# Optimization experiments

Measured on AMD Instinct MI355X. Metric: run time of the kernel, lower is better.

## Reference

```python
import jax, jax.numpy as jnp
import numpy as np

D_MODEL = 256
NUM_HEADS = 8
CURV = 1.0  # Poincare ball curvature c
EPS = 1e-5


def expmap0(v, c):
    # Exponential map at the origin of the Poincare ball.
    sqrt_c = jnp.sqrt(c)
    norm = jnp.sqrt(jnp.clip(jnp.sum(v * v, axis=-1, keepdims=True), 1e-12))
    return jnp.tanh(sqrt_c * norm) * v / (sqrt_c * norm)


def setup_inputs() -> dict:
    key = jax.random.key(0)
    ks = jax.random.split(key, 12)
    B, S, D = 2, 2048, D_MODEL
    s = 1.0 / np.sqrt(D)
    return {
        "x": jax.random.normal(ks[0], (B, S, D), dtype=jnp.float32),
        "Wq": jax.random.normal(ks[1], (D, D), dtype=jnp.float32) * s,
        "bq": jnp.zeros((D,), jnp.float32),
        "Wk": jax.random.normal(ks[2], (D, D), dtype=jnp.float32) * s,
        "bk": jnp.zeros((D,), jnp.float32),
        "Wv": jax.random.normal(ks[3], (D, D), dtype=jnp.float32) * s,
        "bv": jnp.zeros((D,), jnp.float32),
        "Wo": jax.random.normal(ks[4], (D, D), dtype=jnp.float32) * s,
        "bo": jnp.zeros((D,), jnp.float32),
        "Wfc": jax.random.normal(ks[5], (D, D), dtype=jnp.float32) * s,
        "bfc": jnp.zeros((D,), jnp.float32),
    }


def reference(x, Wq, bq, Wk, bk, Wv, bv, Wo, bo, Wfc, bfc):
    B, S, D = x.shape
    H, dh = NUM_HEADS, D // NUM_HEADS
    c = CURV

    def proj(W, b):
        return (x @ W.T + b).reshape(B, S, H, dh).transpose(0, 2, 1, 3)  # [B,H,S,dh]

    q = expmap0(proj(Wq, bq), c)
    k = expmap0(proj(Wk, bk), c)
    v = proj(Wv, bv)

    # Gram quantities; pairwise Poincare distance via closed-form Mobius-add norm.
    qq = jnp.sum(q * q, axis=-1)[..., :, None]          # [B,H,S,1]
    kk = jnp.sum(k * k, axis=-1)[..., None, :]          # [B,H,1,S]
    qk = jnp.einsum("bhsd,bhtd->bhst", q, k)            # [B,H,S,S]

    A = 1.0 - 2.0 * c * qk + c * kk
    Bc = 1.0 - c * qq
    den = 1.0 - 2.0 * c * qk + (c * c) * qq * kk
    num2 = A * A * qq + Bc * Bc * kk - 2.0 * A * Bc * qk  # ||(-q) mobius+ k||^2 * den^2
    n = jnp.sqrt(jnp.clip(num2, 0.0)) / jnp.clip(jnp.abs(den), 1e-12)
    sqrt_c = jnp.sqrt(c)
    dist = (2.0 / sqrt_c) * jnp.arctanh(jnp.clip(sqrt_c * n, 0.0, 1.0 - EPS))

    scores = -dist / np.sqrt(dh)
    attn = jax.nn.softmax(scores, axis=-1)
    out = jnp.einsum("bhst,bhtd->bhsd", attn, v)        # [B,H,S,dh]
    out = out.transpose(0, 2, 1, 3).reshape(B, S, D)
    out = out @ Wo.T + bo
    return out @ Wfc.T + bfc
```

## Files before the change

kernel.cpp:

```cpp
#include <hip/hip_runtime.h>
#include <cstdint>
#include <cstddef>


#define ALPHA 0.17677669529663687f
#define EMIN  -3.1129694f
#define CHI   1.95e-5f

typedef __bf16 bf16x8 __attribute__((ext_vector_type(8)));
typedef float  f32x4  __attribute__((ext_vector_type(4)));

__device__ __forceinline__ float fast_log2(float x) { return __builtin_amdgcn_logf(x); }
__device__ __forceinline__ float fast_exp2(float x) { return __builtin_amdgcn_exp2f(x); }

__device__ __forceinline__ void load_lds16(const void* g, void* l) {
  __builtin_amdgcn_global_load_lds((const __attribute__((address_space(1))) void*)g,
                                   (__attribute__((address_space(3))) void*)l, 16, 0, 0);
}

__global__ __launch_bounds__(256)
void split_all(const float* __restrict__ x, const float* __restrict__ Wq,
               const float* __restrict__ Wk, const float* __restrict__ Wv,
               __bf16* __restrict__ xh, __bf16* __restrict__ xl,
               __bf16* __restrict__ Ws) {
  int g = blockIdx.x * 256 + threadIdx.x;
  const float* src;
  __bf16 *dh, *dl;
  if (g < 131072) {
    src = x + (size_t)g * 8; dh = xh + (size_t)g * 8; dl = xl + (size_t)g * 8;
  } else {
    int e = g - 131072;
    int wsel = e >> 13;
    int inner = (e & 8191) * 8;
    src = (wsel == 0 ? Wq : (wsel == 1 ? Wk : Wv)) + inner;
    dh = Ws + wsel * 131072 + inner;
    dl = Ws + wsel * 131072 + 65536 + inner;
  }
  union { __bf16 h[8]; uint4 u; } ph, pl;
#pragma unroll
  for (int i = 0; i < 2; ++i) {
    float4 v = *(const float4*)(src + i * 4);
    float vv[4] = {v.x, v.y, v.z, v.w};
#pragma unroll
    for (int j = 0; j < 4; ++j) {
      __bf16 hb = (__bf16)vv[j];
      ph.h[i * 4 + j] = hb;
      pl.h[i * 4 + j] = (__bf16)(vv[j] - (float)hb);
    }
  }
  *(uint4*)dh = ph.u;
  *(uint4*)dl = pl.u;
}

__global__ __launch_bounds__(256)
void gemm_qkv_mfma(const __bf16* __restrict__ xh, const __bf16* __restrict__ xl,
                   const __bf16* __restrict__ Ws,
                   const float* __restrict__ bq, const float* __restrict__ bk,
                   const float* __restrict__ bv,
                   float* __restrict__ Qb, float* __restrict__ Kb,
                   float* __restrict__ Vb) {
  const int tid = threadIdx.x, w = tid >> 6, lane = tid & 63;
  const int l15 = lane & 15, lg = lane >> 4;
  const int m0 = blockIdx.x * 64, nb = blockIdx.y;
  const int wsel = nb >> 2;
  const int n256b = (nb & 3) * 64;
  const __bf16* Wh = Ws + wsel * 131072;
  const __bf16* Wl = Wh + 65536;
  const int arow = m0 + w * 16 + l15;
  const __bf16* axh = xh + (size_t)arow * 256 + lg * 8;
  const __bf16* axl = xl + (size_t)arow * 256 + lg * 8;
  f32x4 acc0 = {0,0,0,0}, acc1 = {0,0,0,0}, acc2 = {0,0,0,0}, acc3 = {0,0,0,0};
#pragma unroll
  for (int k0 = 0; k0 < 256; k0 += 32) {
    bf16x8 ah = *(const bf16x8*)(axh + k0);
    bf16x8 al = *(const bf16x8*)(axl + k0);
#pragma unroll
    for (int g = 0; g < 4; ++g) {
      const size_t br = (size_t)(n256b + g * 16 + l15) * 256 + lg * 8 + k0;
      bf16x8 bh = *(const bf16x8*)(Wh + br);
      bf16x8 bl = *(const bf16x8*)(Wl + br);
      f32x4& acc = g == 0 ? acc0 : (g == 1 ? acc1 : (g == 2 ? acc2 : acc3));
      acc = __builtin_amdgcn_mfma_f32_16x16x32_bf16(ah, bh, acc, 0, 0, 0);
      acc = __builtin_amdgcn_mfma_f32_16x16x32_bf16(al, bh, acc, 0, 0, 0);
      acc = __builtin_amdgcn_mfma_f32_16x16x32_bf16(ah, bl, acc, 0, 0, 0);
    }
  }
  const float* bias = wsel == 0 ? bq : (wsel == 1 ? bk : bv);
  float* C = wsel == 0 ? Qb : (wsel == 1 ? Kb : Vb);
#pragma unroll
  for (int g = 0; g < 4; ++g) {
    const f32x4& acc = g == 0 ? acc0 : (g == 1 ? acc1 : (g == 2 ? acc2 : acc3));
    int n256 = n256b + g * 16 + l15;
    float bval = bias[n256];
    int h = n256 >> 5, d = n256 & 31;
#pragma unroll
    for (int r = 0; r < 4; ++r) {
      int m = m0 + w * 16 + lg * 4 + r;
      int b = m >> 11, s = m & 2047;
      C[((size_t)((b << 3) + h) << 16) + (size_t)s * 32 + d] = acc[r] + bval;
    }
  }
}

__global__ __launch_bounds__(256)
void gemm_out_mfma(const __bf16* __restrict__ aoh, const __bf16* __restrict__ aol,
                   const __bf16* __restrict__ Wch, const __bf16* __restrict__ Wcl,
                   const float* __restrict__ bcomb, float* __restrict__ out) {
  const int tid = threadIdx.x, w = tid >> 6, lane = tid & 63;
  const int l15 = lane & 15, lg = lane >> 4;
  const int m0 = blockIdx.x * 64, n0 = blockIdx.y * 64;
  const int arow = m0 + w * 16 + l15;
  const __bf16* axh = aoh + (size_t)arow * 256 + lg * 8;
  const __bf16* axl = aol + (size_t)arow * 256 + lg * 8;
  f32x4 acc0 = {0,0,0,0}, acc1 = {0,0,0,0}, acc2 = {0,0,0,0}, acc3 = {0,0,0,0};
#pragma unroll
  for (int k0 = 0; k0 < 256; k0 += 32) {
    bf16x8 ah = *(const bf16x8*)(axh + k0);
    bf16x8 al = *(const bf16x8*)(axl + k0);
#pragma unroll
    for (int g = 0; g < 4; ++g) {
      const size_t br = (size_t)(n0 + g * 16 + l15) * 256 + lg * 8 + k0;
      bf16x8 bh = *(const bf16x8*)(Wch + br);
      bf16x8 bl = *(const bf16x8*)(Wcl + br);
      f32x4& acc = g == 0 ? acc0 : (g == 1 ? acc1 : (g == 2 ? acc2 : acc3));
      acc = __builtin_amdgcn_mfma_f32_16x16x32_bf16(ah, bh, acc, 0, 0, 0);
      acc = __builtin_amdgcn_mfma_f32_16x16x32_bf16(al, bh, acc, 0, 0, 0);
      acc = __builtin_amdgcn_mfma_f32_16x16x32_bf16(ah, bl, acc, 0, 0, 0);
    }
  }
#pragma unroll
  for (int g = 0; g < 4; ++g) {
    const f32x4& acc = g == 0 ? acc0 : (g == 1 ? acc1 : (g == 2 ? acc2 : acc3));
    int n = n0 + g * 16 + l15;
    float bval = bcomb[n];
#pragma unroll
    for (int r = 0; r < 4; ++r) {
      int m = m0 + w * 16 + lg * 4 + r;
      out[(size_t)m * 256 + n] = acc[r] + bval;
    }
  }
}

__global__ __launch_bounds__(256)
void gemm_nn_small(const float* __restrict__ Afc, const float* __restrict__ Bo,
                   __bf16* __restrict__ Ch, __bf16* __restrict__ Cl) {
  __shared__ float AsT[32][68];
  __shared__ float Bs[32][68];
  const int tid = threadIdx.x;
  const int ty = tid >> 4, tx = tid & 15;
  const int m0 = blockIdx.x * 64;
  const int n0 = blockIdx.y * 64;
  float acc[4][4] = {};
  for (int k0 = 0; k0 < 256; k0 += 32) {
#pragma unroll
    for (int jj = 0; jj < 2; ++jj) {
      int j = tid * 2 + jj;
      {
        int r = j >> 3, c4 = (j & 7) << 2;
        float4 av = *(const float4*)&Afc[(size_t)(m0 + r) * 256 + k0 + c4];
        AsT[c4 + 0][r] = av.x; AsT[c4 + 1][r] = av.y;
        AsT[c4 + 2][r] = av.z; AsT[c4 + 3][r] = av.w;
      }
      {
        int r = j >> 4, c4 = (j & 15) << 2;
        *(float4*)&Bs[r][c4] = *(const float4*)&Bo[(size_t)(k0 + r) * 256 + n0 + c4];
      }
    }
    __syncthreads();
#pragma unroll
    for (int kk = 0; kk < 32; ++kk) {
      float4 a = *(const float4*)&AsT[kk][ty * 4];
      float4 b = *(const float4*)&Bs[kk][tx * 4];
      float av[4] = {a.x, a.y, a.z, a.w};
      float bv[4] = {b.x, b.y, b.z, b.w};
#pragma unroll
      for (int i = 0; i < 4; ++i)
#pragma unroll
        for (int j2 = 0; j2 < 4; ++j2)
          acc[i][j2] = fmaf(av[i], bv[j2], acc[i][j2]);
    }
    __syncthreads();
  }
#pragma unroll
  for (int i = 0; i < 4; ++i) {
    union { __bf16 h[4]; uint2 u; } ph, pl;
#pragma unroll
    for (int j = 0; j < 4; ++j) {
      __bf16 hb = (__bf16)acc[i][j];
      ph.h[j] = hb;
      pl.h[j] = (__bf16)(acc[i][j] - (float)hb);
    }
    size_t off = (size_t)(m0 + ty * 4 + i) * 256 + n0 + tx * 4;
    *(uint2*)(Ch + off) = ph.u;
    *(uint2*)(Cl + off) = pl.u;
  }
}

__global__ __launch_bounds__(256)
void bcomb_k(const float* __restrict__ Wfc, const float* __restrict__ bo,
             const float* __restrict__ bfc, float* __restrict__ bcomb) {
  __shared__ float red[256];
  int r = threadIdx.x >> 4, c = threadIdx.x & 15;
  int row = blockIdx.x * 16 + r;
  float s = 0.0f;
  for (int k = c; k < 256; k += 16) s = fmaf(Wfc[(size_t)row * 256 + k], bo[k], s);
  red[threadIdx.x] = s;
  __syncthreads();
  if (c == 0) {
    float t = 0.0f;
#pragma unroll
    for (int i = 0; i < 16; ++i) t += red[r * 16 + i];
    bcomb[row] = t + bfc[row];
  }
}

__global__ __launch_bounds__(256)
void prep_qk(const float* __restrict__ Qf, const float* __restrict__ Kf,
             __bf16* __restrict__ Qbf, __bf16* __restrict__ Kbf,
             float4* __restrict__ qtab4, float4* __restrict__ ktab4) {
  int idx = blockIdx.x * 256 + threadIdx.x;
  const bool isQ = idx < 32768;
  const int i2 = isQ ? idx : idx - 32768;
  const float* src = (isQ ? Qf : Kf) + (size_t)i2 * 32;
  __bf16* dst = (isQ ? Qbf : Kbf) + (size_t)i2 * 32;
  float v[32];
  float ss = 0.0f;
#pragma unroll
  for (int i = 0; i < 8; ++i) {
    float4 v4 = *(const float4*)&src[i * 4];
    v[i*4+0] = v4.x; v[i*4+1] = v4.y; v[i*4+2] = v4.z; v[i*4+3] = v4.w;
    ss = fmaf(v4.x, v4.x, ss); ss = fmaf(v4.y, v4.y, ss);
    ss = fmaf(v4.z, v4.z, ss); ss = fmaf(v4.w, v4.w, ss);
  }
  ss = fmaxf(ss, 1e-12f);
  float x  = sqrtf(ss);
  float ex = fast_exp2(-2.8853900817779268f * x);
  float opex = 1.0f + ex;
  float th = (1.0f - ex) / opex;
  float sc = th / x;
  float qq = th * th;
  float Bv = 4.0f * ex / (opex * opex);
  float lgB = 2.0f - 2.8853900817779268f * x - 2.0f * fast_log2(opex);
  if (isQ) qtab4[i2] = float4{qq, ALPHA * lgB, Bv, 0.0f};
  else     ktab4[i2] = float4{qq, Bv, ALPHA * lgB, 0.0f};
  union { __bf16 h[8]; uint4 u; } pk;
#pragma unroll
  for (int blk = 0; blk < 4; ++blk) {
#pragma unroll
    for (int j = 0; j < 8; ++j) pk.h[j] = (__bf16)(v[blk * 8 + j] * sc);
    *(uint4*)(dst + blk * 8) = pk.u;
  }
}

__global__ __launch_bounds__(256)
void prep_vt(const float* __restrict__ Vf, __bf16* __restrict__ Vt) {
  int g = blockIdx.x * 256 + threadIdx.x;
  int bh = g >> 13, rem = g & 8191;
  int tb = rem >> 5, dh = rem & 31;
  const float* src = Vf + (((size_t)bh * 2048 + tb * 8) * 32) + dh;
  union { __bf16 h[8]; uint4 u; } pk;
#pragma unroll
  for (int e = 0; e < 8; ++e) pk.h[e] = (__bf16)src[e * 32];
  *(uint4*)(Vt + ((size_t)bh * 32 + dh) * 2048 + tb * 8) = pk.u;
}

__global__ __launch_bounds__(256)
void vsum_k(const __bf16* __restrict__ Vt, float* __restrict__ Vsum) {
  int g = blockIdx.x * 256 + threadIdx.x;
  int bh = g >> 11, rem = g & 2047;
  int t32 = rem >> 5, dh = rem & 31;
  const __bf16* src = Vt + ((size_t)bh * 32 + dh) * 2048 + t32 * 32;
  float s = 0.0f;
#pragma unroll
  for (int i = 0; i < 4; ++i) {
    bf16x8 v = *(const bf16x8*)&src[i * 8];
#pragma unroll
    for (int j = 0; j < 8; ++j) s += (float)v[j];
  }
  Vsum[((size_t)bh * 64 + t32) * 32 + dh] = s;
}

__global__ __launch_bounds__(256)
void attn_mfma(const __bf16* __restrict__ Qbf, const __bf16* __restrict__ Kbf,
               const __bf16* __restrict__ Vt,  const float4* __restrict__ qtab4,
               const float4* __restrict__ ktab4, const float* __restrict__ Vsum,
               float* __restrict__ PN, float* __restrict__ PD) {
  __shared__ __bf16 Kst[2][2048];
  __shared__ float4 Tst[2][64];
  __shared__ __bf16 Pt[4][16][72];
  const int tid = threadIdx.x;
  const int wid = tid >> 6, lane = tid & 63;
  const int l15 = lane & 15, lg = lane >> 4;
  const int tc = blockIdx.y, bh = blockIdx.z;
  const int sblk = blockIdx.x;
  const int s0 = sblk * 64 + wid * 16;

  bf16x8 qfrag = *(const bf16x8*)(Qbf + ((size_t)bh * 2048 + s0 + l15) * 32 + lg * 8);
  float4 qt = qtab4[bh * 2048 + s0 + l15];
  const float qq = qt.x, Bq = qt.z;
  const float eminRow = EMIN - qt.y;
  const float wclipf = (float)(__bf16)fast_exp2(eminRow);
  float wrow[4];
#pragma unroll
  for (int r = 0; r < 4; ++r)
    wrow[r] = (float)(__bf16)fast_exp2(EMIN - qtab4[bh * 2048 + s0 + lg * 4 + r].y);

  const __bf16* Kbase = Kbf + ((size_t)bh << 16);
  const __bf16* Vbase = Vt + ((size_t)bh << 16);
  const float4* Tbase = ktab4 + bh * 2048;
  const float*  VsBase = Vsum + (size_t)bh * 64 * 32;
  __bf16* Pw = &Pt[wid][0][0];

  f32x4 accO0 = {0.f, 0.f, 0.f, 0.f};
  f32x4 accO1 = {0.f, 0.f, 0.f, 0.f};
  float den = 0.0f;
  const f32x4 zero = {0.f, 0.f, 0.f, 0.f};
  const int tbeg = tc * 512;
  const int stag = sblk & 7;

  const int slot = wid * 64 + lane;
  const int gch = slot ^ ((slot >> 2) & 3);

  {
    const int t0 = tbeg + ((stag & 7) << 6);
    load_lds16(Kbase + (size_t)t0 * 32 + gch * 8, &Kst[0][wid * 512]);
    if (wid == 0) load_lds16(Tbase + t0 + lane, &Tst[0][0]);
  }
  int cur = 0;

  for (int i = 0; i < 8; ++i) {
    __syncthreads();
    if (i < 7) {
      const int tn = tbeg + (((i + 1 + stag) & 7) << 6);
      load_lds16(Kbase + (size_t)tn * 32 + gch * 8, &Kst[cur ^ 1][wid * 512]);
      if (wid == 0) load_lds16(Tbase + tn + lane, &Tst[cur ^ 1][0]);
    }
    const int t0 = tbeg + (((i + stag) & 7) << 6);
    const __bf16* Kc = &Kst[cur][0];
    const float4* Tc = &Tst[cur][0];

#pragma unroll
    for (int h = 0; h < 2; ++h) {
      f32x4 S[2];
      bool ok = true;
#pragma unroll
      for (int s2 = 0; s2 < 2; ++s2) {
        const int sub = h * 2 + s2;
        const int R = sub * 16 + l15;
        const int slotR = R * 4 + (lg ^ (R & 3));
        bf16x8 kfrag = *(const bf16x8*)&Kc[slotR * 8];
        f32x4 Sv = __builtin_amdgcn_mfma_f32_16x16x32_bf16(kfrag, qfrag, zero, 0, 0, 0);
        S[s2] = Sv;
        const int tk = sub * 16 + lg * 4;
#pragma unroll
        for (int r = 0; r < 4; ++r) {
          float2 T2 = *(const float2*)&Tc[tk + r];
          float d = fmaf(qq, T2.x, 1.0f) - (Sv[r] + Sv[r]);
          ok &= (fmaf(-CHI, d, Bq * T2.y) <= 0.0f);
        }
      }
      if (__all((int)ok)) {
        const int ti32 = (t0 >> 5) + h;
        float vsA = VsBase[ti32 * 32 + l15];
        float vsB = VsBase[ti32 * 32 + 16 + l15];
        den += 8.0f * wclipf;
#pragma unroll
        for (int r = 0; r < 4; ++r) {
          accO0[r] = fmaf(wrow[r], vsA, accO0[r]);
          accO1[r] = fmaf(wrow[r], vsB, accO1[r]);
        }
      } else {
#pragma unroll
        for (int s2 = 0; s2 < 2; ++s2) {
          const int sub = h * 2 + s2;
          const int tk = sub * 16 + lg * 4;
          f32x4 Sv = S[s2];
          float w[4];
#pragma unroll
          for (int r = 0; r < 4; ++r) {
            float4 T = Tc[tk + r];
            float qk2 = Sv[r] + Sv[r];
            float u = (qq + T.x) - qk2;
            float d = fmaf(qq, T.x, 1.0f) - qk2;
            float p = fmaxf(u * d, 0.0f);
            float sq = sqrtf(p);
            float m = fmaf(2.0f, sq, u + d);
            float e = fmaf(-ALPHA, fast_log2(m), T.z);
            e = fmaxf(e, eminRow);
            w[r] = fast_exp2(e);
          }
          den += (w[0] + w[1]) + (w[2] + w[3]);
          union { __bf16 hh[4]; uint2 u2; } pk;
          pk.hh[0] = (__bf16)w[0]; pk.hh[1] = (__bf16)w[1];
          pk.hh[2] = (__bf16)w[2]; pk.hh[3] = (__bf16)w[3];
          *(uint2*)&Pw[l15 * 72 + sub * 16 + lg * 4] = pk.u2;
        }
        bf16x8 pfrag = *(const bf16x8*)&Pw[l15 * 72 + h * 32 + lg * 8];
        bf16x8 v0 = *(const bf16x8*)(Vbase + (size_t)l15 * 2048 + t0 + h * 32 + lg * 8);
        bf16x8 v1 = *(const bf16x8*)(Vbase + (size_t)(16 + l15) * 2048 + t0 + h * 32 + lg * 8);
        accO0 = __builtin_amdgcn_mfma_f32_16x16x32_bf16(pfrag, v0, accO0, 0, 0, 0);
        accO1 = __builtin_amdgcn_mfma_f32_16x16x32_bf16(pfrag, v1, accO1, 0, 0, 0);
      }
    }
    cur ^= 1;
  }
  den += __shfl_xor(den, 16);
  den += __shfl_xor(den, 32);
  size_t pbase = ((size_t)tc * 16 + bh) * 2048;
  if (lg == 0) PD[pbase + s0 + l15] = den;
#pragma unroll
  for (int r = 0; r < 4; ++r) {
    int sl = lg * 4 + r;
    size_t row = (pbase + s0 + sl) * 32;
    PN[row + l15]      = accO0[r];
    PN[row + 16 + l15] = accO1[r];
  }
}

__global__ __launch_bounds__(256)
void combine4(const float* __restrict__ PN, const float* __restrict__ PD,
              __bf16* __restrict__ AOh, __bf16* __restrict__ AOl) {
  int idx = blockIdx.x * 256 + threadIdx.x;
  int bh = idx >> 11, s = idx & 2047;
  int b = bh >> 3, h = bh & 7;
  float den = 0.0f;
#pragma unroll
  for (int c = 0; c < 4; ++c) den += PD[((size_t)c * 16 + bh) * 2048 + s];
  float r = 1.0f / den;
  size_t ob = ((size_t)b * 2048 + s) * 256 + h * 32;
#pragma unroll
  for (int i = 0; i < 8; ++i) {
    float4 sum = {0.0f, 0.0f, 0.0f, 0.0f};
#pragma unroll
    for (int c = 0; c < 4; ++c) {
      float4 v = *(const float4*)&PN[((((size_t)c * 16 + bh) * 2048 + s) * 32) + i * 4];
      sum.x += v.x; sum.y += v.y; sum.z += v.z; sum.w += v.w;
    }
    float vv[4] = {sum.x * r, sum.y * r, sum.z * r, sum.w * r};
    union { __bf16 h4[4]; uint2 u; } ph, pl;
#pragma unroll
    for (int j = 0; j < 4; ++j) {
      __bf16 hb = (__bf16)vv[j];
      ph.h4[j] = hb;
      pl.h4[j] = (__bf16)(vv[j] - (float)hb);
    }
    *(uint2*)(AOh + ob + i * 4) = ph.u;
    *(uint2*)(AOl + ob + i * 4) = pl.u;
  }
}

extern "C" void kernel_launch(void* const* d_in, const int* in_sizes, int n_in,
                              void* d_out, int out_size, void* d_ws, size_t ws_size,
                              hipStream_t stream) {
  const float* x   = (const float*)d_in[0];
  const float* Wq  = (const float*)d_in[1];
  const float* bq  = (const float*)d_in[2];
  const float* Wk  = (const float*)d_in[3];
  const float* bk  = (const float*)d_in[4];
  const float* Wv  = (const float*)d_in[5];
  const float* bv  = (const float*)d_in[6];
  const float* Wo  = (const float*)d_in[7];
  const float* bo  = (const float*)d_in[8];
  const float* Wfc = (const float*)d_in[9];
  const float* bfc = (const float*)d_in[10];

  float* ws = (float*)d_ws;
  float* Qb  = ws;
  float* Kb  = ws + (1 << 20);
  float* Vb  = ws + (2 << 20);
  __bf16* Qbf = (__bf16*)(ws + (3 << 20));
  __bf16* Kbf = (__bf16*)(ws + (3 << 20) + (1 << 19));
  __bf16* Vtb = (__bf16*)(ws + (4 << 20));
  float4* qtab4 = (float4*)(ws + (4 << 20) + (1 << 19));
  float4* ktab4 = (float4*)(ws + (4 << 20) + (1 << 19) + (1 << 17));
  float*  Vsum  = ws + (4 << 20) + (1 << 19) + (2 << 17);
  __bf16* Wch   = (__bf16*)(ws + (4 << 20) + (1 << 19) + (2 << 17) + (1 << 15));
  __bf16* Wcl   = Wch + 65536;
  float*  bcomb = ws + (4 << 20) + (1 << 19) + (2 << 17) + (1 << 15) + (1 << 16);
  __bf16* xh = (__bf16*)(ws + (5 << 20));
  __bf16* xl = (__bf16*)(ws + (5 << 20) + (1 << 19));
  __bf16* Wsplit = (__bf16*)(ws + (6 << 20));
  float* PN = ws + (6 << 20) + (1 << 18);
  float* PD = PN + (4 << 20);
  __bf16* AOh = (__bf16*)ws;
  __bf16* AOl = (__bf16*)(ws + (1 << 19));

  dim3 blk(256);
  split_all<<<dim3(608), blk, 0, stream>>>(x, Wq, Wk, Wv, xh, xl, Wsplit);
  gemm_qkv_mfma<<<dim3(64, 12), blk, 0, stream>>>(xh, xl, Wsplit, bq, bk, bv, Qb, Kb, Vb);
  prep_qk<<<dim3(256), blk, 0, stream>>>(Qb, Kb, Qbf, Kbf, qtab4, ktab4);
  prep_vt<<<dim3(512), blk, 0, stream>>>(Vb, Vtb);
  vsum_k<<<dim3(128), blk, 0, stream>>>(Vtb, Vsum);
  gemm_nn_small<<<dim3(4, 4), blk, 0, stream>>>(Wfc, Wo, Wch, Wcl);
  bcomb_k<<<dim3(16), blk, 0, stream>>>(Wfc, bo, bfc, bcomb);
  attn_mfma<<<dim3(32, 4, 16), blk, 0, stream>>>(Qbf, Kbf, Vtb, qtab4, ktab4, Vsum, PN, PD);
  combine4<<<dim3(128), blk, 0, stream>>>(PN, PD, AOh, AOl);
  gemm_out_mfma<<<dim3(64, 4), blk, 0, stream>>>(AOh, AOl, Wch, Wcl, bcomb, (float*)d_out);
}
```

Before: 123.3 us.

## Merge prep kernels and use per-head key bounds for skip test

After: 109.6 us. 1.13x faster.

```diff
diff --git a/kernel.cpp b/kernel.cpp
--- a/kernel.cpp
+++ b/kernel.cpp
@@ -6,6 +6,7 @@
 #define ALPHA 0.17677669529663687f
 #define EMIN  -3.1129694f
 #define CHI   1.95e-5f
+#define NEG_INV_2CHI -25641.026f
 
 typedef __bf16 bf16x8 __attribute__((ext_vector_type(8)));
 typedef float  f32x4  __attribute__((ext_vector_type(4)));
@@ -19,37 +20,107 @@
 }
 
 __global__ __launch_bounds__(256)
-void split_all(const float* __restrict__ x, const float* __restrict__ Wq,
-               const float* __restrict__ Wk, const float* __restrict__ Wv,
-               __bf16* __restrict__ xh, __bf16* __restrict__ xl,
-               __bf16* __restrict__ Ws) {
-  int g = blockIdx.x * 256 + threadIdx.x;
-  const float* src;
-  __bf16 *dh, *dl;
-  if (g < 131072) {
-    src = x + (size_t)g * 8; dh = xh + (size_t)g * 8; dl = xl + (size_t)g * 8;
+void k1_misc(const float* __restrict__ x,   const float* __restrict__ Wq,
+             const float* __restrict__ Wk,  const float* __restrict__ Wv,
+             const float* __restrict__ Wfc, const float* __restrict__ Wo,
+             const float* __restrict__ bo,  const float* __restrict__ bfc,
+             __bf16* __restrict__ xh, __bf16* __restrict__ xl,
+             __bf16* __restrict__ Ws, __bf16* __restrict__ Wch,
+             __bf16* __restrict__ Wcl, float* __restrict__ bcomb) {
+  __shared__ float sh[2 * 32 * 68];
+  const int bx = blockIdx.x, tid = threadIdx.x;
+  if (bx < 16) {
+    float (*AsT)[68] = (float(*)[68])sh;
+    float (*Bs)[68]  = (float(*)[68])(sh + 32 * 68);
+    const int ty = tid >> 4, tx = tid & 15;
+    const int m0 = (bx >> 2) * 64, n0 = (bx & 3) * 64;
+    float acc[4][4] = {};
+    for (int k0 = 0; k0 < 256; k0 += 32) {
+#pragma unroll
+      for (int jj = 0; jj < 2; ++jj) {
+        int j = tid * 2 + jj;
+        {
+          int r = j >> 3, c4 = (j & 7) << 2;
+          float4 av = *(const float4*)&Wfc[(size_t)(m0 + r) * 256 + k0 + c4];
+          AsT[c4 + 0][r] = av.x; AsT[c4 + 1][r] = av.y;
+          AsT[c4 + 2][r] = av.z; AsT[c4 + 3][r] = av.w;
+        }
+        {
+          int r = j >> 4, c4 = (j & 15) << 2;
+          *(float4*)&Bs[r][c4] = *(const float4*)&Wo[(size_t)(k0 + r) * 256 + n0 + c4];
+        }
+      }
+      __syncthreads();
+#pragma unroll
+      for (int kk = 0; kk < 32; ++kk) {
+        float4 a = *(const float4*)&AsT[kk][ty * 4];
+        float4 b = *(const float4*)&Bs[kk][tx * 4];
+        float av[4] = {a.x, a.y, a.z, a.w};
+        float bv[4] = {b.x, b.y, b.z, b.w};
+#pragma unroll
+        for (int i = 0; i < 4; ++i)
+#pragma unroll
+          for (int j2 = 0; j2 < 4; ++j2)
+            acc[i][j2] = fmaf(av[i], bv[j2], acc[i][j2]);
+      }
+      __syncthreads();
+    }
+#pragma unroll
+    for (int i = 0; i < 4; ++i) {
+      union { __bf16 h[4]; uint2 u; } ph, pl;
+#pragma unroll
+      for (int j = 0; j < 4; ++j) {
+        __bf16 hb = (__bf16)acc[i][j];
+        ph.h[j] = hb;
+        pl.h[j] = (__bf16)(acc[i][j] - (float)hb);
+      }
+      size_t off = (size_t)(m0 + ty * 4 + i) * 256 + n0 + tx * 4;
+      *(uint2*)(Wch + off) = ph.u;
+      *(uint2*)(Wcl + off) = pl.u;
+    }
+  } else if (bx < 32) {
+    float* red = sh;
+    int r = tid >> 4, c = tid & 15;
+    int row = (bx - 16) * 16 + r;
+    float s = 0.0f;
+    for (int k = c; k < 256; k += 16) s = fmaf(Wfc[(size_t)row * 256 + k], bo[k], s);
+    red[tid] = s;
+    __syncthreads();
+    if (c == 0) {
+      float t = 0.0f;
+#pragma unroll
+      for (int i = 0; i < 16; ++i) t += red[r * 16 + i];
+      bcomb[row] = t + bfc[row];
+    }
   } else {
-    int e = g - 131072;
-    int wsel = e >> 13;
-    int inner = (e & 8191) * 8;
-    src = (wsel == 0 ? Wq : (wsel == 1 ? Wk : Wv)) + inner;
-    dh = Ws + wsel * 131072 + inner;
-    dl = Ws + wsel * 131072 + 65536 + inner;
-  }
-  union { __bf16 h[8]; uint4 u; } ph, pl;
-#pragma unroll
-  for (int i = 0; i < 2; ++i) {
-    float4 v = *(const float4*)(src + i * 4);
-    float vv[4] = {v.x, v.y, v.z, v.w};
-#pragma unroll
-    for (int j = 0; j < 4; ++j) {
-      __bf16 hb = (__bf16)vv[j];
-      ph.h[i * 4 + j] = hb;
-      pl.h[i * 4 + j] = (__bf16)(vv[j] - (float)hb);
-    }
-  }
-  *(uint4*)dh = ph.u;
-  *(uint4*)dl = pl.u;
+    int g = (bx - 32) * 256 + tid;
+    const float* src;
+    __bf16 *dh, *dl;
+    if (g < 131072) {
+      src = x + (size_t)g * 8; dh = xh + (size_t)g * 8; dl = xl + (size_t)g * 8;
+    } else {
+      int e = g - 131072;
+      int wsel = e >> 13;
+      int inner = (e & 8191) * 8;
+      src = (wsel == 0 ? Wq : (wsel == 1 ? Wk : Wv)) + inner;
+      dh = Ws + wsel * 131072 + inner;
+      dl = Ws + wsel * 131072 + 65536 + inner;
+    }
+    union { __bf16 h[8]; uint4 u; } ph, pl;
+#pragma unroll
+    for (int i = 0; i < 2; ++i) {
+      float4 v = *(const float4*)(src + i * 4);
+      float vv[4] = {v.x, v.y, v.z, v.w};
+#pragma unroll
+      for (int j = 0; j < 4; ++j) {
+        __bf16 hb = (__bf16)vv[j];
+        ph.h[i * 4 + j] = hb;
+        pl.h[i * 4 + j] = (__bf16)(vv[j] - (float)hb);
+      }
+    }
+    *(uint4*)dh = ph.u;
+    *(uint4*)dl = pl.u;
+  }
 }
 
 __global__ __launch_bounds__(256)
@@ -103,190 +174,87 @@
 }
 
 __global__ __launch_bounds__(256)
-void gemm_out_mfma(const __bf16* __restrict__ aoh, const __bf16* __restrict__ aol,
-                   const __bf16* __restrict__ Wch, const __bf16* __restrict__ Wcl,
-                   const float* __restrict__ bcomb, float* __restrict__ out) {
-  const int tid = threadIdx.x, w = tid >> 6, lane = tid & 63;
-  const int l15 = lane & 15, lg = lane >> 4;
-  const int m0 = blockIdx.x * 64, n0 = blockIdx.y * 64;
-  const int arow = m0 + w * 16 + l15;
-  const __bf16* axh = aoh + (size_t)arow * 256 + lg * 8;
-  const __bf16* axl = aol + (size_t)arow * 256 + lg * 8;
-  f32x4 acc0 = {0,0,0,0}, acc1 = {0,0,0,0}, acc2 = {0,0,0,0}, acc3 = {0,0,0,0};
-#pragma unroll
-  for (int k0 = 0; k0 < 256; k0 += 32) {
-    bf16x8 ah = *(const bf16x8*)(axh + k0);
-    bf16x8 al = *(const bf16x8*)(axl + k0);
-#pragma unroll
-    for (int g = 0; g < 4; ++g) {
-      const size_t br = (size_t)(n0 + g * 16 + l15) * 256 + lg * 8 + k0;
-      bf16x8 bh = *(const bf16x8*)(Wch + br);
-      bf16x8 bl = *(const bf16x8*)(Wcl + br);
-      f32x4& acc = g == 0 ? acc0 : (g == 1 ? acc1 : (g == 2 ? acc2 : acc3));
-      acc = __builtin_amdgcn_mfma_f32_16x16x32_bf16(ah, bh, acc, 0, 0, 0);
-      acc = __builtin_amdgcn_mfma_f32_16x16x32_bf16(al, bh, acc, 0, 0, 0);
-      acc = __builtin_amdgcn_mfma_f32_16x16x32_bf16(ah, bl, acc, 0, 0, 0);
-    }
-  }
-#pragma unroll
-  for (int g = 0; g < 4; ++g) {
-    const f32x4& acc = g == 0 ? acc0 : (g == 1 ? acc1 : (g == 2 ? acc2 : acc3));
-    int n = n0 + g * 16 + l15;
-    float bval = bcomb[n];
-#pragma unroll
-    for (int r = 0; r < 4; ++r) {
-      int m = m0 + w * 16 + lg * 4 + r;
-      out[(size_t)m * 256 + n] = acc[r] + bval;
-    }
-  }
-}
-
-__global__ __launch_bounds__(256)
-void gemm_nn_small(const float* __restrict__ Afc, const float* __restrict__ Bo,
-                   __bf16* __restrict__ Ch, __bf16* __restrict__ Cl) {
-  __shared__ float AsT[32][68];
-  __shared__ float Bs[32][68];
-  const int tid = threadIdx.x;
-  const int ty = tid >> 4, tx = tid & 15;
-  const int m0 = blockIdx.x * 64;
-  const int n0 = blockIdx.y * 64;
-  float acc[4][4] = {};
-  for (int k0 = 0; k0 < 256; k0 += 32) {
-#pragma unroll
-    for (int jj = 0; jj < 2; ++jj) {
-      int j = tid * 2 + jj;
-      {
-        int r = j >> 3, c4 = (j & 7) << 2;
-        float4 av = *(const float4*)&Afc[(size_t)(m0 + r) * 256 + k0 + c4];
-        AsT[c4 + 0][r] = av.x; AsT[c4 + 1][r] = av.y;
-        AsT[c4 + 2][r] = av.z; AsT[c4 + 3][r] = av.w;
-      }
-      {
-        int r = j >> 4, c4 = (j & 15) << 2;
-        *(float4*)&Bs[r][c4] = *(const float4*)&Bo[(size_t)(k0 + r) * 256 + n0 + c4];
-      }
-    }
-    __syncthreads();
-#pragma unroll
-    for (int kk = 0; kk < 32; ++kk) {
-      float4 a = *(const float4*)&AsT[kk][ty * 4];
-      float4 b = *(const float4*)&Bs[kk][tx * 4];
-      float av[4] = {a.x, a.y, a.z, a.w};
-      float bv[4] = {b.x, b.y, b.z, b.w};
-#pragma unroll
-      for (int i = 0; i < 4; ++i)
-#pragma unroll
-        for (int j2 = 0; j2 < 4; ++j2)
-          acc[i][j2] = fmaf(av[i], bv[j2], acc[i][j2]);
-    }
-    __syncthreads();
-  }
-#pragma unroll
-  for (int i = 0; i < 4; ++i) {
-    union { __bf16 h[4]; uint2 u; } ph, pl;
-#pragma unroll
-    for (int j = 0; j < 4; ++j) {
-      __bf16 hb = (__bf16)acc[i][j];
-      ph.h[j] = hb;
-      pl.h[j] = (__bf16)(acc[i][j] - (float)hb);
-    }
-    size_t off = (size_t)(m0 + ty * 4 + i) * 256 + n0 + tx * 4;
-    *(uint2*)(Ch + off) = ph.u;
-    *(uint2*)(Cl + off) = pl.u;
-  }
-}
-
-__global__ __launch_bounds__(256)
-void bcomb_k(const float* __restrict__ Wfc, const float* __restrict__ bo,
-             const float* __restrict__ bfc, float* __restrict__ bcomb) {
-  __shared__ float red[256];
-  int r = threadIdx.x >> 4, c = threadIdx.x & 15;
-  int row = blockIdx.x * 16 + r;
-  float s = 0.0f;
-  for (int k = c; k < 256; k += 16) s = fmaf(Wfc[(size_t)row * 256 + k], bo[k], s);
-  red[threadIdx.x] = s;
-  __syncthreads();
-  if (c == 0) {
-    float t = 0.0f;
-#pragma unroll
-    for (int i = 0; i < 16; ++i) t += red[r * 16 + i];
-    bcomb[row] = t + bfc[row];
-  }
-}
-
-__global__ __launch_bounds__(256)
-void prep_qk(const float* __restrict__ Qf, const float* __restrict__ Kf,
+void k3_prep(const float* __restrict__ Qf, const float* __restrict__ Kf,
+             const float* __restrict__ Vf,
              __bf16* __restrict__ Qbf, __bf16* __restrict__ Kbf,
-             float4* __restrict__ qtab4, float4* __restrict__ ktab4) {
-  int idx = blockIdx.x * 256 + threadIdx.x;
-  const bool isQ = idx < 32768;
-  const int i2 = isQ ? idx : idx - 32768;
-  const float* src = (isQ ? Qf : Kf) + (size_t)i2 * 32;
-  __bf16* dst = (isQ ? Qbf : Kbf) + (size_t)i2 * 32;
-  float v[32];
-  float ss = 0.0f;
-#pragma unroll
-  for (int i = 0; i < 8; ++i) {
-    float4 v4 = *(const float4*)&src[i * 4];
-    v[i*4+0] = v4.x; v[i*4+1] = v4.y; v[i*4+2] = v4.z; v[i*4+3] = v4.w;
-    ss = fmaf(v4.x, v4.x, ss); ss = fmaf(v4.y, v4.y, ss);
-    ss = fmaf(v4.z, v4.z, ss); ss = fmaf(v4.w, v4.w, ss);
-  }
-  ss = fmaxf(ss, 1e-12f);
-  float x  = sqrtf(ss);
-  float ex = fast_exp2(-2.8853900817779268f * x);
-  float opex = 1.0f + ex;
-  float th = (1.0f - ex) / opex;
-  float sc = th / x;
-  float qq = th * th;
-  float Bv = 4.0f * ex / (opex * opex);
-  float lgB = 2.0f - 2.8853900817779268f * x - 2.0f * fast_log2(opex);
-  if (isQ) qtab4[i2] = float4{qq, ALPHA * lgB, Bv, 0.0f};
-  else     ktab4[i2] = float4{qq, Bv, ALPHA * lgB, 0.0f};
-  union { __bf16 h[8]; uint4 u; } pk;
-#pragma unroll
-  for (int blk = 0; blk < 4; ++blk) {
-#pragma unroll
-    for (int j = 0; j < 8; ++j) pk.h[j] = (__bf16)(v[blk * 8 + j] * sc);
-    *(uint4*)(dst + blk * 8) = pk.u;
-  }
-}
-
-__global__ __launch_bounds__(256)
-void prep_vt(const float* __restrict__ Vf, __bf16* __restrict__ Vt) {
-  int g = blockIdx.x * 256 + threadIdx.x;
-  int bh = g >> 13, rem = g & 8191;
-  int tb = rem >> 5, dh = rem & 31;
-  const float* src = Vf + (((size_t)bh * 2048 + tb * 8) * 32) + dh;
-  union { __bf16 h[8]; uint4 u; } pk;
-#pragma unroll
-  for (int e = 0; e < 8; ++e) pk.h[e] = (__bf16)src[e * 32];
-  *(uint4*)(Vt + ((size_t)bh * 32 + dh) * 2048 + tb * 8) = pk.u;
-}
-
-__global__ __launch_bounds__(256)
-void vsum_k(const __bf16* __restrict__ Vt, float* __restrict__ Vsum) {
-  int g = blockIdx.x * 256 + threadIdx.x;
-  int bh = g >> 11, rem = g & 2047;
-  int t32 = rem >> 5, dh = rem & 31;
-  const __bf16* src = Vt + ((size_t)bh * 32 + dh) * 2048 + t32 * 32;
-  float s = 0.0f;
-#pragma unroll
-  for (int i = 0; i < 4; ++i) {
-    bf16x8 v = *(const bf16x8*)&src[i * 8];
-#pragma unroll
-    for (int j = 0; j < 8; ++j) s += (float)v[j];
-  }
-  Vsum[((size_t)bh * 64 + t32) * 32 + dh] = s;
+             __bf16* __restrict__ Vt,
+             float4* __restrict__ qtab4, float4* __restrict__ ktab4,
+             float* __restrict__ Vsum, float2* __restrict__ Kred) {
+  __shared__ float2 red2[256];
+  const int bx = blockIdx.x, tid = threadIdx.x;
+  if (bx < 256) {
+    int idx = bx * 256 + tid;
+    const bool isQ = idx < 32768;
+    const int i2 = isQ ? idx : idx - 32768;
+    const float* src = (isQ ? Qf : Kf) + (size_t)i2 * 32;
+    __bf16* dst = (isQ ? Qbf : Kbf) + (size_t)i2 * 32;
+    float v[32];
+    float ss = 0.0f;
+#pragma unroll
+    for (int i = 0; i < 8; ++i) {
+      float4 v4 = *(const float4*)&src[i * 4];
+      v[i*4+0] = v4.x; v[i*4+1] = v4.y; v[i*4+2] = v4.z; v[i*4+3] = v4.w;
+      ss = fmaf(v4.x, v4.x, ss); ss = fmaf(v4.y, v4.y, ss);
+      ss = fmaf(v4.z, v4.z, ss); ss = fmaf(v4.w, v4.w, ss);
+    }
+    ss = fmaxf(ss, 1e-12f);
+    float x  = sqrtf(ss);
+    float ex = fast_exp2(-2.8853900817779268f * x);
+    float opex = 1.0f + ex;
+    float th = (1.0f - ex) / opex;
+    float sc = th / x;
+    float qq = th * th;
+    float Bv = 4.0f * ex / (opex * opex);
+    float lgB = 2.0f - 2.8853900817779268f * x - 2.0f * fast_log2(opex);
+    if (isQ) qtab4[i2] = float4{qq, ALPHA * lgB, Bv, 0.0f};
+    else     ktab4[i2] = float4{qq, Bv, ALPHA * lgB, 0.0f};
+    union { __bf16 h[8]; uint4 u; } pk;
+#pragma unroll
+    for (int blk = 0; blk < 4; ++blk) {
+#pragma unroll
+      for (int j = 0; j < 8; ++j) pk.h[j] = (__bf16)(v[blk * 8 + j] * sc);
+      *(uint4*)(dst + blk * 8) = pk.u;
+    }
+    if (!isQ) {
+      red2[tid] = float2{qq, Bv};
+      __syncthreads();
+      for (int s = 128; s > 0; s >>= 1) {
+        if (tid < s) {
+          red2[tid].x = fminf(red2[tid].x, red2[tid + s].x);
+          red2[tid].y = fmaxf(red2[tid].y, red2[tid + s].y);
+        }
+        __syncthreads();
+      }
+      if (tid == 0) Kred[bx - 128] = red2[0];
+    }
+  } else if (bx < 768) {
+    int g = (bx - 256) * 256 + tid;
+    int bh = g >> 13, rem = g & 8191;
+    int tb = rem >> 5, dh = rem & 31;
+    const float* src = Vf + (((size_t)bh * 2048 + tb * 8) * 32) + dh;
+    union { __bf16 h[8]; uint4 u; } pk;
+#pragma unroll
+    for (int e = 0; e < 8; ++e) pk.h[e] = (__bf16)src[e * 32];
+    *(uint4*)(Vt + ((size_t)bh * 32 + dh) * 2048 + tb * 8) = pk.u;
+  } else {
+    int g = (bx - 768) * 256 + tid;
+    int bh = g >> 11, rem = g & 2047;
+    int t32 = rem >> 5, dh = rem & 31;
+    const float* src = Vf + (((size_t)bh * 2048 + t32 * 32) * 32) + dh;
+    float s = 0.0f;
+#pragma unroll
+    for (int j = 0; j < 32; ++j) s += src[j * 32];
+    Vsum[((size_t)bh * 64 + t32) * 32 + dh] = s;
+  }
 }
 
 __global__ __launch_bounds__(256)
 void attn_mfma(const __bf16* __restrict__ Qbf, const __bf16* __restrict__ Kbf,
                const __bf16* __restrict__ Vt,  const float4* __restrict__ qtab4,
                const float4* __restrict__ ktab4, const float* __restrict__ Vsum,
+               const float2* __restrict__ Kred,
                float* __restrict__ PN, float* __restrict__ PD) {
   __shared__ __bf16 Kst[2][2048];
-  __shared__ float4 Tst[2][64];
   __shared__ __bf16 Pt[4][16][72];
   const int tid = threadIdx.x;
   const int wid = tid >> 6, lane = tid & 63;
@@ -305,9 +273,19 @@
   for (int r = 0; r < 4; ++r)
     wrow[r] = (float)(__bf16)fast_exp2(EMIN - qtab4[bh * 2048 + s0 + lg * 4 + r].y);
 
+  float kkmin = 1.0f, bkmax = 0.0f;
+#pragma unroll
+  for (int j = 0; j < 8; ++j) {
+    float2 kr = Kred[bh * 8 + j];
+    kkmin = fminf(kkmin, kr.x);
+    bkmax = fmaxf(bkmax, kr.y);
+  }
+  const float thr_all = fmaf(0.5f * qq, kkmin,
+                             fmaf(Bq * NEG_INV_2CHI, bkmax, 0.5f));
+
   const __bf16* Kbase = Kbf + ((size_t)bh << 16);
   const __bf16* Vbase = Vt + ((size_t)bh << 16);
-  const float4* Tbase = ktab4 + bh * 2048;
+  const float4* Tk = ktab4 + bh * 2048;
   const float*  VsBase = Vsum + (size_t)bh * 64 * 32;
   __bf16* Pw = &Pt[wid][0][0];
 
@@ -324,7 +302,6 @@
   {
     const int t0 = tbeg + ((stag & 7) << 6);
     load_lds16(Kbase + (size_t)t0 * 32 + gch * 8, &Kst[0][wid * 512]);
-    if (wid == 0) load_lds16(Tbase + t0 + lane, &Tst[0][0]);
   }
   int cur = 0;
 
@@ -333,11 +310,9 @@
     if (i < 7) {
       const int tn = tbeg + (((i + 1 + stag) & 7) << 6);
       load_lds16(Kbase + (size_t)tn * 32 + gch * 8, &Kst[cur ^ 1][wid * 512]);
-      if (wid == 0) load_lds16(Tbase + tn + lane, &Tst[cur ^ 1][0]);
     }
     const int t0 = tbeg + (((i + stag) & 7) << 6);
     const __bf16* Kc = &Kst[cur][0];
-    const float4* Tc = &Tst[cur][0];
 
 #pragma unroll
     for (int h = 0; h < 2; ++h) {
@@ -351,13 +326,8 @@
         bf16x8 kfrag = *(const bf16x8*)&Kc[slotR * 8];
         f32x4 Sv = __builtin_amdgcn_mfma_f32_16x16x32_bf16(kfrag, qfrag, zero, 0, 0, 0);
         S[s2] = Sv;
-        const int tk = sub * 16 + lg * 4;
-#pragma unroll
-        for (int r = 0; r < 4; ++r) {
-          float2 T2 = *(const float2*)&Tc[tk + r];
-          float d = fmaf(qq, T2.x, 1.0f) - (Sv[r] + Sv[r]);
-          ok &= (fmaf(-CHI, d, Bq * T2.y) <= 0.0f);
-        }
+        float m = fmaxf(fmaxf(Sv[0], Sv[1]), fmaxf(Sv[2], Sv[3]));
+        ok &= (m <= thr_all);
       }
       if (__all((int)ok)) {
         const int ti32 = (t0 >> 5) + h;
@@ -373,12 +343,12 @@
 #pragma unroll
         for (int s2 = 0; s2 < 2; ++s2) {
           const int sub = h * 2 + s2;
-          const int tk = sub * 16 + lg * 4;
+          const int tk = t0 + sub * 16 + lg * 4;
           f32x4 Sv = S[s2];
           float w[4];
 #pragma unroll
           for (int r = 0; r < 4; ++r) {
-            float4 T = Tc[tk + r];
+            float4 T = Tk[tk + r];
             float qk2 = Sv[r] + Sv[r];
             float u = (qq + T.x) - qk2;
             float d = fmaf(qq, T.x, 1.0f) - qk2;
@@ -449,6 +419,45 @@
   }
 }
 
+__global__ __launch_bounds__(256)
+void gemm_out_mfma(const __bf16* __restrict__ aoh, const __bf16* __restrict__ aol,
+                   const __bf16* __restrict__ Wch, const __bf16* __restrict__ Wcl,
+                   const float* __restrict__ bcomb, float* __restrict__ out) {
+  const int tid = threadIdx.x, w = tid >> 6, lane = tid & 63;
+  const int l15 = lane & 15, lg = lane >> 4;
+  const int m0 = blockIdx.x * 64, n0 = blockIdx.y * 64;
+  const int arow = m0 + w * 16 + l15;
+  const __bf16* axh = aoh + (size_t)arow * 256 + lg * 8;
+  const __bf16* axl = aol + (size_t)arow * 256 + lg * 8;
+  f32x4 acc0 = {0,0,0,0}, acc1 = {0,0,0,0}, acc2 = {0,0,0,0}, acc3 = {0,0,0,0};
+#pragma unroll
+  for (int k0 = 0; k0 < 256; k0 += 32) {
+    bf16x8 ah = *(const bf16x8*)(axh + k0);
+    bf16x8 al = *(const bf16x8*)(axl + k0);
+#pragma unroll
+    for (int g = 0; g < 4; ++g) {
+      const size_t br = (size_t)(n0 + g * 16 + l15) * 256 + lg * 8 + k0;
+      bf16x8 bh = *(const bf16x8*)(Wch + br);
+      bf16x8 bl = *(const bf16x8*)(Wcl + br);
+      f32x4& acc = g == 0 ? acc0 : (g == 1 ? acc1 : (g == 2 ? acc2 : acc3));
+      acc = __builtin_amdgcn_mfma_f32_16x16x32_bf16(ah, bh, acc, 0, 0, 0);
+      acc = __builtin_amdgcn_mfma_f32_16x16x32_bf16(al, bh, acc, 0, 0, 0);
+      acc = __builtin_amdgcn_mfma_f32_16x16x32_bf16(ah, bl, acc, 0, 0, 0);
+    }
+  }
+#pragma unroll
+  for (int g = 0; g < 4; ++g) {
+    const f32x4& acc = g == 0 ? acc0 : (g == 1 ? acc1 : (g == 2 ? acc2 : acc3));
+    int n = n0 + g * 16 + l15;
+    float bval = bcomb[n];
+#pragma unroll
+    for (int r = 0; r < 4; ++r) {
+      int m = m0 + w * 16 + lg * 4 + r;
+      out[(size_t)m * 256 + n] = acc[r] + bval;
+    }
+  }
+}
+
 extern "C" void kernel_launch(void* const* d_in, const int* in_sizes, int n_in,
                               void* d_out, int out_size, void* d_ws, size_t ws_size,
                               hipStream_t stream) {
@@ -474,9 +483,10 @@
   float4* qtab4 = (float4*)(ws + (4 << 20) + (1 << 19));
   float4* ktab4 = (float4*)(ws + (4 << 20) + (1 << 19) + (1 << 17));
   float*  Vsum  = ws + (4 << 20) + (1 << 19) + (2 << 17);
-  __bf16* Wch   = (__bf16*)(ws + (4 << 20) + (1 << 19) + (2 << 17) + (1 << 15));
+  __bf16* Wch   = (__bf16*)(Vsum + (1 << 15));
   __bf16* Wcl   = Wch + 65536;
-  float*  bcomb = ws + (4 << 20) + (1 << 19) + (2 << 17) + (1 << 15) + (1 << 16);
+  float*  bcomb = Vsum + (1 << 15) + (1 << 16);
+  float2* Kred  = (float2*)(bcomb + 256);
   __bf16* xh = (__bf16*)(ws + (5 << 20));
   __bf16* xl = (__bf16*)(ws + (5 << 20) + (1 << 19));
   __bf16* Wsplit = (__bf16*)(ws + (6 << 20));
@@ -486,14 +496,15 @@
   __bf16* AOl = (__bf16*)(ws + (1 << 19));
 
   dim3 blk(256);
-  split_all<<<dim3(608), blk, 0, stream>>>(x, Wq, Wk, Wv, xh, xl, Wsplit);
-  gemm_qkv_mfma<<<dim3(64, 12), blk, 0, stream>>>(xh, xl, Wsplit, bq, bk, bv, Qb, Kb, Vb);
-  prep_qk<<<dim3(256), blk, 0, stream>>>(Qb, Kb, Qbf, Kbf, qtab4, ktab4);
-  prep_vt<<<dim3(512), blk, 0, stream>>>(Vb, Vtb);
-  vsum_k<<<dim3(128), blk, 0, stream>>>(Vtb, Vsum);
-  gemm_nn_small<<<dim3(4, 4), blk, 0, stream>>>(Wfc, Wo, Wch, Wcl);
-  bcomb_k<<<dim3(16), blk, 0, stream>>>(Wfc, bo, bfc, bcomb);
-  attn_mfma<<<dim3(32, 4, 16), blk, 0, stream>>>(Qbf, Kbf, Vtb, qtab4, ktab4, Vsum, PN, PD);
+  k1_misc<<<dim3(640), blk, 0, stream>>>(x, Wq, Wk, Wv, Wfc, Wo, bo, bfc,
+                                         xh, xl, Wsplit, Wch, Wcl, bcomb);
+  gemm_qkv_mfma<<<dim3(64, 12), blk, 0, stream>>>(xh, xl, Wsplit, bq, bk, bv,
+                                                  Qb, Kb, Vb);
+  k3_prep<<<dim3(896), blk, 0, stream>>>(Qb, Kb, Vb, Qbf, Kbf, Vtb,
+                                         qtab4, ktab4, Vsum, Kred);
+  attn_mfma<<<dim3(32, 4, 16), blk, 0, stream>>>(Qbf, Kbf, Vtb, qtab4, ktab4,
+                                                 Vsum, Kred, PN, PD);
   combine4<<<dim3(128), blk, 0, stream>>>(PN, PD, AOh, AOl);
-  gemm_out_mfma<<<dim3(64, 4), blk, 0, stream>>>(AOh, AOl, Wch, Wcl, bcomb, (float*)d_out);
-}
+  gemm_out_mfma<<<dim3(64, 4), blk, 0, stream>>>(AOh, AOl, Wch, Wcl, bcomb,
+                                                 (float*)d_out);
+}
```
